# Performance work log

Hardware: AMD Instinct MI355X
Metric: run time of the kernel (lower is better)

Reference implementation:

```python
import jax, jax.numpy as jnp
import numpy as np

NUM_HEADS = 4


def setup_inputs() -> dict:
    key = jax.random.key(0)
    k1, k2, k3 = jax.random.split(key, 3)
    B, NN, C = 1, 256, 128
    x = jax.random.normal(k1, (B, NN, C), dtype=jnp.float32)
    # Linear(d_model, 4*d_model, bias=False); stored as (in, out) for x @ W_w
    W_w = jax.random.normal(k2, (C, 4 * C), dtype=jnp.float32) * (C ** -0.5)
    # proj = Linear(d_model, d_model) with bias; stored as (in, out)
    W_proj = jax.random.normal(k3, (C, C), dtype=jnp.float32) * (C ** -0.5)
    b_proj = jnp.zeros((C,), dtype=jnp.float32)
    return {"x": x, "W_w": W_w, "W_proj": W_proj, "b_proj": b_proj}


def reference(x, W_w, W_proj, b_proj):
    B, NN, C = x.shape
    H = NUM_HEADS
    D = C // H
    scale = D ** -0.5
    # qkv-style projection: (B, NN, 4, H, D) -> (4, B, H, NN, D)
    w = (x @ W_w).reshape(B, NN, 4, H, D).transpose(2, 0, 3, 1, 4)
    a, b, c, v = w[0], w[1], w[2], w[3]
    AB = jnp.einsum('bhid,bhjd->bhij', a, b) * scale
    CD = jnp.einsum('bhid,bhkd->bhik', a, c) * scale
    EF = jnp.einsum('bhjd,bhkd->bhjk', b, c) * scale
    # Triplet scores: (B, H, NN, NN, NN)
    A_ijk = AB[..., :, :, None] + CD[..., :, None, :] + EF[..., None, :, :]
    e = jnp.exp(A_ijk)
    # Normalize over (i, j) for each k, per original sum(dim=(-2,-3))
    norm = jnp.clip(e.sum(axis=(-2, -3), keepdims=True), 1e-6, None)
    en = e / norm
    x1 = jnp.einsum('bhijk,bhjd->bhid', en, v)
    x2 = jnp.einsum('bhijk,bhkd->bhid', en, v)
    out = (x1 * x2).transpose(0, 2, 1, 3).reshape(B, NN, C)
    return out @ W_proj + b_proj
```

## Files before the change

### kernel.cpp

```cpp
#include <hip/hip_runtime.h>
#include <hip/hip_bf16.h>


constexpr size_t OFF_W     = 0;
constexpr size_t OFF_P     = 131072;
constexpr size_t OFF_Q     = OFF_P + 262144;
constexpr size_t OFF_RT    = OFF_Q + 262144;
constexpr size_t OFF_T     = OFF_RT + 262144;
constexpr size_t OFF_S     = OFF_T + 524288;
constexpr size_t OFF_NORMP = OFF_S + 524288;

__global__ __launch_bounds__(256) void k_w(const float* __restrict__ x,
                                           const float* __restrict__ Ww,
                                           float* __restrict__ w,
                                           const float* __restrict__ bp,
                                           float* __restrict__ out) {
    __shared__ __align__(16) float As[1152];
    __shared__ __align__(16) float Bs[1152];
    int j0 = blockIdx.x * 32, i0 = blockIdx.y * 32;
    int t = threadIdx.x, tx = t & 15, ty = t >> 4, r = t >> 3, g = t & 7;
    {
        int oidx = (blockIdx.y * 16 + blockIdx.x) * 256 + t;
        out[oidx] = bp[oidx & 127];
    }
    float4 a4 = *(const float4*)&x[(size_t)(i0 + r) * 128 + g * 4];
    float4 b4 = *(const float4*)&Ww[(size_t)r * 512 + j0 + g * 4];
    float a00 = 0, a01 = 0, a10 = 0, a11 = 0;
    for (int kc = 0; kc < 128; kc += 32) {
        As[(g * 4 + 0) * 36 + r] = a4.x; As[(g * 4 + 1) * 36 + r] = a4.y;
        As[(g * 4 + 2) * 36 + r] = a4.z; As[(g * 4 + 3) * 36 + r] = a4.w;
        *(float4*)&Bs[r * 36 + g * 4] = b4;
        __syncthreads();
        if (kc + 32 < 128) {
            a4 = *(const float4*)&x[(size_t)(i0 + r) * 128 + kc + 32 + g * 4];
            b4 = *(const float4*)&Ww[(size_t)(kc + 32 + r) * 512 + j0 + g * 4];
        }
#pragma unroll
        for (int kk = 0; kk < 32; kk++) {
            float2 av = *(float2*)&As[kk * 36 + ty * 2];
            float2 bv = *(float2*)&Bs[kk * 36 + tx * 2];
            a00 += av.x * bv.x; a01 += av.x * bv.y;
            a10 += av.y * bv.x; a11 += av.y * bv.y;
        }
        __syncthreads();
    }
    *(float2*)&w[(size_t)(i0 + ty * 2) * 512 + j0 + tx * 2] = make_float2(a00, a01);
    *(float2*)&w[(size_t)(i0 + ty * 2 + 1) * 512 + j0 + tx * 2] = make_float2(a10, a11);
}

__global__ __launch_bounds__(256, 2) void k_T(const float* __restrict__ w,
                                              float* __restrict__ P,
                                              float* __restrict__ Q,
                                              float* __restrict__ Rt,
                                              float* __restrict__ T,
                                              float* __restrict__ normp) {
    __shared__ __align__(16) float aT[1152];
    __shared__ __align__(16) float cT[1152];
    __shared__ __align__(16) float bT[1152];
    __shared__ __align__(16) float PsT[1152];
    __shared__ __align__(16) float RsT[1152];
    int h = blockIdx.z >> 1, jh = blockIdx.z & 1;
    int k0 = blockIdx.x * 32, i0 = blockIdx.y * 32;
    int jc0 = jh * 128;
    size_t hb = (size_t)h * 65536;
    int t = threadIdx.x, tx = t & 15, ty = t >> 4, r = t >> 3, g = t & 7;
    const float sc = 0.17677669529663687f;

    float4 av = *(const float4*)&w[(size_t)(i0 + r) * 512 + h * 32 + g * 4];
    aT[(g * 4 + 0) * 36 + r] = av.x; aT[(g * 4 + 1) * 36 + r] = av.y;
    aT[(g * 4 + 2) * 36 + r] = av.z; aT[(g * 4 + 3) * 36 + r] = av.w;
    float4 cv = *(const float4*)&w[(size_t)(k0 + r) * 512 + 256 + h * 32 + g * 4];
    cT[(g * 4 + 0) * 36 + r] = cv.x; cT[(g * 4 + 1) * 36 + r] = cv.y;
    cT[(g * 4 + 2) * 36 + r] = cv.z; cT[(g * 4 + 3) * 36 + r] = cv.w;
    float4 bv = *(const float4*)&w[(size_t)(jc0 + r) * 512 + 128 + h * 32 + g * 4];
    __syncthreads();

    float2 a_tx[32], c_tx[32];
#pragma unroll
    for (int d = 0; d < 32; d++) {
        a_tx[d] = *(float2*)&aT[d * 36 + 2 * tx];
        c_tx[d] = *(float2*)&cT[d * 36 + 2 * tx];
    }

    float dq00 = 0, dq01 = 0, dq10 = 0, dq11 = 0;
#pragma unroll
    for (int d = 0; d < 32; d++) {
        float2 a2 = *(float2*)&aT[d * 36 + 2 * ty];
        float2 c2 = c_tx[d];
        dq00 += a2.x * c2.x; dq01 += a2.x * c2.y;
        dq10 += a2.y * c2.x; dq11 += a2.y * c2.y;
    }
    float q00 = __expf(sc * dq00), q01 = __expf(sc * dq01);
    float q10 = __expf(sc * dq10), q11 = __expf(sc * dq11);
    if (jh == 0) {
        *(float2*)&Q[hb + (size_t)(i0 + ty * 2) * 256 + k0 + tx * 2] = make_float2(q00, q01);
        *(float2*)&Q[hb + (size_t)(i0 + ty * 2 + 1) * 256 + k0 + tx * 2] = make_float2(q10, q11);
    }

    const bool wP = (k0 == 0), wR = (blockIdx.y == 0);
    float acc00 = 0, acc01 = 0, acc10 = 0, acc11 = 0;
    for (int jc = jc0; jc < jc0 + 128; jc += 32) {
        bT[(g * 4 + 0) * 36 + r] = bv.x; bT[(g * 4 + 1) * 36 + r] = bv.y;
        bT[(g * 4 + 2) * 36 + r] = bv.z; bT[(g * 4 + 3) * 36 + r] = bv.w;
        __syncthreads();
        if (jc + 32 < jc0 + 128)
            bv = *(const float4*)&w[(size_t)(jc + 32 + r) * 512 + 128 + h * 32 + g * 4];
        float dp00 = 0, dp01 = 0, dp10 = 0, dp11 = 0;
        float dr00 = 0, dr01 = 0, dr10 = 0, dr11 = 0;
#pragma unroll
        for (int d = 0; d < 32; d++) {
            float2 b2 = *(float2*)&bT[d * 36 + 2 * ty];
            float2 a2 = a_tx[d];
            float2 c2 = c_tx[d];
            dp00 += b2.x * a2.x; dp01 += b2.x * a2.y;
            dp10 += b2.y * a2.x; dp11 += b2.y * a2.y;
            dr00 += b2.x * c2.x; dr01 += b2.x * c2.y;
            dr10 += b2.y * c2.x; dr11 += b2.y * c2.y;
        }
        float p00 = __expf(sc * dp00), p01 = __expf(sc * dp01);
        float p10 = __expf(sc * dp10), p11 = __expf(sc * dp11);
        float r00 = __expf(sc * dr00), r01 = __expf(sc * dr01);
        float r10 = __expf(sc * dr10), r11 = __expf(sc * dr11);
        *(float2*)&PsT[(2 * tx + 0) * 36 + 2 * ty] = make_float2(p00, p10);
        *(float2*)&PsT[(2 * tx + 1) * 36 + 2 * ty] = make_float2(p01, p11);
        *(float2*)&RsT[(2 * tx + 0) * 36 + 2 * ty] = make_float2(r00, r10);
        *(float2*)&RsT[(2 * tx + 1) * 36 + 2 * ty] = make_float2(r01, r11);
        if (wP) {
            *(float2*)&P[hb + (size_t)(i0 + tx * 2 + 0) * 256 + jc + ty * 2] = make_float2(p00, p10);
            *(float2*)&P[hb + (size_t)(i0 + tx * 2 + 1) * 256 + jc + ty * 2] = make_float2(p01, p11);
        }
        if (wR) {
            *(float2*)&Rt[hb + (size_t)(k0 + tx * 2 + 0) * 256 + jc + ty * 2] = make_float2(r00, r10);
            *(float2*)&Rt[hb + (size_t)(k0 + tx * 2 + 1) * 256 + jc + ty * 2] = make_float2(r01, r11);
        }
        __syncthreads();
#pragma unroll
        for (int q = 0; q < 8; q++) {
            float4 pA = *(float4*)&PsT[(2 * ty + 0) * 36 + 4 * q];
            float4 pB = *(float4*)&PsT[(2 * ty + 1) * 36 + 4 * q];
            float4 rA = *(float4*)&RsT[(2 * tx + 0) * 36 + 4 * q];
            float4 rB = *(float4*)&RsT[(2 * tx + 1) * 36 + 4 * q];
            acc00 += pA.x * rA.x + pA.y * rA.y + pA.z * rA.z + pA.w * rA.w;
            acc01 += pA.x * rB.x + pA.y * rB.y + pA.z * rB.z + pA.w * rB.w;
            acc10 += pB.x * rA.x + pB.y * rA.y + pB.z * rA.z + pB.w * rA.w;
            acc11 += pB.x * rB.x + pB.y * rB.y + pB.z * rB.z + pB.w * rB.w;
        }
    }
    float* Tp = T + (size_t)jh * 262144;
    *(float2*)&Tp[hb + (size_t)(i0 + ty * 2) * 256 + k0 + tx * 2] = make_float2(acc00, acc01);
    *(float2*)&Tp[hb + (size_t)(i0 + ty * 2 + 1) * 256 + k0 + tx * 2] = make_float2(acc10, acc11);
    __syncthreads();
    float* red = PsT;
    red[ty * 34 + tx * 2]     = q00 * acc00 + q10 * acc10;
    red[ty * 34 + tx * 2 + 1] = q01 * acc01 + q11 * acc11;
    __syncthreads();
    if (t < 32) {
        float s = 0.f;
#pragma unroll
        for (int m = 0; m < 16; m++) s += red[m * 34 + t];
        normp[h * 4096 + (jh * 8 + blockIdx.y) * 256 + k0 + t] = s;
    }
}

__global__ __launch_bounds__(256, 2) void k_S(const float* __restrict__ Q,
                                              const float* __restrict__ Rt,
                                              const float* __restrict__ normp,
                                              float* __restrict__ S) {
    __shared__ __align__(16) float AsT[1152];
    __shared__ __align__(16) float BsT[1152];
    __shared__ float rn_s[256];
    int h = blockIdx.z >> 1, kh = blockIdx.z & 1;
    int j0 = blockIdx.x * 32, i0 = blockIdx.y * 32;
    int kc0 = kh * 128;
    size_t hb = (size_t)h * 65536;
    int t = threadIdx.x, tx = t & 15, ty = t >> 4, r = t >> 3, g = t & 7;
    {
        float s = 0.f;
#pragma unroll
        for (int ib = 0; ib < 16; ib++) s += normp[h * 4096 + ib * 256 + t];
        rn_s[t] = 1.f / fmaxf(s, 1e-6f);
    }
    float4 a4 = *(const float4*)&Q[hb + (size_t)(i0 + r) * 256 + kc0 + g * 4];
    float4 b4 = *(const float4*)&Rt[hb + (size_t)(kc0 + r) * 256 + j0 + g * 4];
    __syncthreads();
    float a00 = 0, a01 = 0, a10 = 0, a11 = 0;
    for (int kc = kc0; kc < kc0 + 128; kc += 32) {
        float4 rn4 = *(float4*)&rn_s[kc + g * 4];
        float4 as4;
        as4.x = a4.x * rn4.x; as4.y = a4.y * rn4.y;
        as4.z = a4.z * rn4.z; as4.w = a4.w * rn4.w;
        *(float4*)&AsT[r * 36 + g * 4] = as4;
        BsT[(g * 4 + 0) * 36 + r] = b4.x;
        BsT[(g * 4 + 1) * 36 + r] = b4.y;
        BsT[(g * 4 + 2) * 36 + r] = b4.z;
        BsT[(g * 4 + 3) * 36 + r] = b4.w;
        __syncthreads();
        if (kc + 32 < kc0 + 128) {
            a4 = *(const float4*)&Q[hb + (size_t)(i0 + r) * 256 + kc + 32 + g * 4];
            b4 = *(const float4*)&Rt[hb + (size_t)(kc + 32 + r) * 256 + j0 + g * 4];
        }
#pragma unroll
        for (int q = 0; q < 8; q++) {
            float4 aA = *(float4*)&AsT[(2 * ty + 0) * 36 + 4 * q];
            float4 aB = *(float4*)&AsT[(2 * ty + 1) * 36 + 4 * q];
            float4 bA = *(float4*)&BsT[(2 * tx + 0) * 36 + 4 * q];
            float4 bB = *(float4*)&BsT[(2 * tx + 1) * 36 + 4 * q];
            a00 += aA.x * bA.x + aA.y * bA.y + aA.z * bA.z + aA.w * bA.w;
            a01 += aA.x * bB.x + aA.y * bB.y + aA.z * bB.z + aA.w * bB.w;
            a10 += aB.x * bA.x + aB.y * bA.y + aB.z * bA.z + aB.w * bA.w;
            a11 += aB.x * bB.x + aB.y * bB.y + aB.z * bB.z + aB.w * bB.w;
        }
        __syncthreads();
    }
    float* Sp = S + (size_t)kh * 262144;
    *(float2*)&Sp[hb + (size_t)(i0 + ty * 2) * 256 + j0 + tx * 2] = make_float2(a00, a01);
    *(float2*)&Sp[hb + (size_t)(i0 + ty * 2 + 1) * 256 + j0 + tx * 2] = make_float2(a10, a11);
}

__global__ __launch_bounds__(256) void k_x1x2(
    const float* __restrict__ P, const float* __restrict__ Q,
    const float* __restrict__ S, const float* __restrict__ T,
    const float* __restrict__ normp, const float* __restrict__ w,
    const float* __restrict__ Wp, float* __restrict__ out) {
    int h = blockIdx.y;
    int i0 = blockIdx.x * 4;
    size_t hb = (size_t)h * 65536;
    __shared__ __align__(16) float wp[1024];
    __shared__ __align__(16) float wq[1024];
    __shared__ __align__(16) float vT[8320];
    __shared__ float rn_s[256];
    __shared__ float ys[144];
    int t = threadIdx.x;
    {
        float s = 0.f;
#pragma unroll
        for (int ib = 0; ib < 16; ib++) s += normp[h * 4096 + ib * 256 + t];
        rn_s[t] = 1.f / fmaxf(s, 1e-6f);
    }
    __syncthreads();
    {
        int rr = t >> 6, jj = (t & 63) * 4;
        size_t o = hb + (size_t)(i0 + rr) * 256 + jj;
        float4 p4  = *(const float4*)&P[o];
        float4 s4a = *(const float4*)&S[o];
        float4 s4b = *(const float4*)&S[o + 262144];
        float4 q4  = *(const float4*)&Q[o];
        float4 t4a = *(const float4*)&T[o];
        float4 t4b = *(const float4*)&T[o + 262144];
        float4 rn4 = *(float4*)&rn_s[jj];
        float4 wpv, wqv;
        wpv.x = p4.x * (s4a.x + s4b.x); wpv.y = p4.y * (s4a.y + s4b.y);
        wpv.z = p4.z * (s4a.z + s4b.z); wpv.w = p4.w * (s4a.w + s4b.w);
        wqv.x = q4.x * (t4a.x + t4b.x) * rn4.x;
        wqv.y = q4.y * (t4a.y + t4b.y) * rn4.y;
        wqv.z = q4.z * (t4a.z + t4b.z) * rn4.z;
        wqv.w = q4.w * (t4a.w + t4b.w) * rn4.w;
        *(float4*)&wp[rr * 256 + jj] = wpv;
        *(float4*)&wq[rr * 256 + jj] = wqv;
    }
#pragma unroll
    for (int m = 0; m < 8; m++) {
        int jj = m * 32 + (t >> 3);
        int dd = (t & 7) * 4;
        float4 v4 = *(const float4*)&w[(size_t)jj * 512 + 384 + h * 32 + dd];
        vT[(dd + 0) * 260 + jj] = v4.x;
        vT[(dd + 1) * 260 + jj] = v4.y;
        vT[(dd + 2) * 260 + jj] = v4.z;
        vT[(dd + 3) * 260 + jj] = v4.w;
    }
    __syncthreads();
    int d = t & 31, rl = (t >> 5) & 3, jh2 = t >> 7;
    int jbase = jh2 * 128;
    float x1 = 0.f, x2 = 0.f;
#pragma unroll
    for (int q = 0; q < 32; q++) {
        int j = jbase + 4 * q;
        float4 wp4 = *(float4*)&wp[rl * 256 + j];
        float4 wq4 = *(float4*)&wq[rl * 256 + j];
        float4 v4  = *(float4*)&vT[d * 260 + j];
        x1 += wp4.x * v4.x + wp4.y * v4.y + wp4.z * v4.z + wp4.w * v4.w;
        x2 += wq4.x * v4.x + wq4.y * v4.y + wq4.z * v4.z + wq4.w * v4.w;
    }
    __syncthreads();
    float* redx = wp;
    float* redy = wq;
    redx[t] = x1;
    redy[t] = x2;
    float* Wps = vT;
#pragma unroll
    for (int m = 0; m < 4; m++) {
        int idx = m * 256 + t;
        int k = idx >> 5, n = (idx & 31) * 4;
        *(float4*)&Wps[k * 128 + n] = *(const float4*)&Wp[(size_t)(h * 32 + k) * 128 + n];
    }
    __syncthreads();
    if (t < 128) {
        float x1t = redx[t] + redx[t + 128];
        float x2t = redy[t] + redy[t + 128];
        ys[rl * 33 + d] = x1t * x2t;
    }
    __syncthreads();
    int n = t & 127, ti = t >> 7;
    float acc0 = 0.f, acc1 = 0.f;
#pragma unroll
    for (int k = 0; k < 32; k++) {
        float wv = Wps[k * 128 + n];
        acc0 += ys[(ti + 0) * 33 + k] * wv;
        acc1 += ys[(ti + 2) * 33 + k] * wv;
    }
    atomicAdd(&out[(size_t)(i0 + ti + 0) * 128 + n], acc0);
    atomicAdd(&out[(size_t)(i0 + ti + 2) * 128 + n], acc1);
}

extern "C" void kernel_launch(void* const* d_in, const int* in_sizes, int n_in,
                              void* d_out, int out_size, void* d_ws, size_t ws_size,
                              hipStream_t stream) {
    const float* x      = (const float*)d_in[0];
    const float* W_w    = (const float*)d_in[1];
    const float* W_proj = (const float*)d_in[2];
    const float* b_proj = (const float*)d_in[3];
    float* out = (float*)d_out;
    float* ws  = (float*)d_ws;

    float* w     = ws + OFF_W;
    float* P     = ws + OFF_P;
    float* Q     = ws + OFF_Q;
    float* Rt    = ws + OFF_RT;
    float* T     = ws + OFF_T;
    float* S     = ws + OFF_S;
    float* normp = ws + OFF_NORMP;

    k_w<<<dim3(16, 8), 256, 0, stream>>>(x, W_w, w, b_proj, out);
    k_T<<<dim3(8, 8, 8), 256, 0, stream>>>(w, P, Q, Rt, T, normp);
    k_S<<<dim3(8, 8, 8), 256, 0, stream>>>(Q, Rt, normp, S);
    k_x1x2<<<dim3(64, 4), 256, 0, stream>>>(P, Q, S, T, normp, w, W_proj, out);
}
```

Before: 39.77 us.

## Fuse S matmul into x1x2 kernel, computing S rows on the fly

Removes the separate k_S GEMM launch and its S workspace round-trip. Each x1x2 block now computes its 4 rows of S = (Q*rn) @ Rt directly, splitting K across four thread groups and reducing through shared memory. It saves one launch and the S global writes and reads. In exchange every block streams the full per-head Rt (256x256) from global or L2 with little reuse, across 256 blocks.

```diff
diff --git a/kernel.cpp b/kernel.cpp
--- a/kernel.cpp
+++ b/kernel.cpp
@@ -7,8 +7,7 @@
 constexpr size_t OFF_Q     = OFF_P + 262144;
 constexpr size_t OFF_RT    = OFF_Q + 262144;
 constexpr size_t OFF_T     = OFF_RT + 262144;
-constexpr size_t OFF_S     = OFF_T + 524288;
-constexpr size_t OFF_NORMP = OFF_S + 524288;
+constexpr size_t OFF_NORMP = OFF_T + 524288;
 
 __global__ __launch_bounds__(256) void k_w(const float* __restrict__ x,
                                            const float* __restrict__ Ww,
@@ -162,73 +161,20 @@
     }
 }
 
-__global__ __launch_bounds__(256, 2) void k_S(const float* __restrict__ Q,
-                                              const float* __restrict__ Rt,
-                                              const float* __restrict__ normp,
-                                              float* __restrict__ S) {
-    __shared__ __align__(16) float AsT[1152];
-    __shared__ __align__(16) float BsT[1152];
-    __shared__ float rn_s[256];
-    int h = blockIdx.z >> 1, kh = blockIdx.z & 1;
-    int j0 = blockIdx.x * 32, i0 = blockIdx.y * 32;
-    int kc0 = kh * 128;
-    size_t hb = (size_t)h * 65536;
-    int t = threadIdx.x, tx = t & 15, ty = t >> 4, r = t >> 3, g = t & 7;
-    {
-        float s = 0.f;
-#pragma unroll
-        for (int ib = 0; ib < 16; ib++) s += normp[h * 4096 + ib * 256 + t];
-        rn_s[t] = 1.f / fmaxf(s, 1e-6f);
-    }
-    float4 a4 = *(const float4*)&Q[hb + (size_t)(i0 + r) * 256 + kc0 + g * 4];
-    float4 b4 = *(const float4*)&Rt[hb + (size_t)(kc0 + r) * 256 + j0 + g * 4];
-    __syncthreads();
-    float a00 = 0, a01 = 0, a10 = 0, a11 = 0;
-    for (int kc = kc0; kc < kc0 + 128; kc += 32) {
-        float4 rn4 = *(float4*)&rn_s[kc + g * 4];
-        float4 as4;
-        as4.x = a4.x * rn4.x; as4.y = a4.y * rn4.y;
-        as4.z = a4.z * rn4.z; as4.w = a4.w * rn4.w;
-        *(float4*)&AsT[r * 36 + g * 4] = as4;
-        BsT[(g * 4 + 0) * 36 + r] = b4.x;
-        BsT[(g * 4 + 1) * 36 + r] = b4.y;
-        BsT[(g * 4 + 2) * 36 + r] = b4.z;
-        BsT[(g * 4 + 3) * 36 + r] = b4.w;
-        __syncthreads();
-        if (kc + 32 < kc0 + 128) {
-            a4 = *(const float4*)&Q[hb + (size_t)(i0 + r) * 256 + kc + 32 + g * 4];
-            b4 = *(const float4*)&Rt[hb + (size_t)(kc + 32 + r) * 256 + j0 + g * 4];
-        }
-#pragma unroll
-        for (int q = 0; q < 8; q++) {
-            float4 aA = *(float4*)&AsT[(2 * ty + 0) * 36 + 4 * q];
-            float4 aB = *(float4*)&AsT[(2 * ty + 1) * 36 + 4 * q];
-            float4 bA = *(float4*)&BsT[(2 * tx + 0) * 36 + 4 * q];
-            float4 bB = *(float4*)&BsT[(2 * tx + 1) * 36 + 4 * q];
-            a00 += aA.x * bA.x + aA.y * bA.y + aA.z * bA.z + aA.w * bA.w;
-            a01 += aA.x * bB.x + aA.y * bB.y + aA.z * bB.z + aA.w * bB.w;
-            a10 += aB.x * bA.x + aB.y * bA.y + aB.z * bA.z + aB.w * bA.w;
-            a11 += aB.x * bB.x + aB.y * bB.y + aB.z * bB.z + aB.w * bB.w;
-        }
-        __syncthreads();
-    }
-    float* Sp = S + (size_t)kh * 262144;
-    *(float2*)&Sp[hb + (size_t)(i0 + ty * 2) * 256 + j0 + tx * 2] = make_float2(a00, a01);
-    *(float2*)&Sp[hb + (size_t)(i0 + ty * 2 + 1) * 256 + j0 + tx * 2] = make_float2(a10, a11);
-}
-
-__global__ __launch_bounds__(256) void k_x1x2(
+__global__ __launch_bounds__(256) void k_x1x2S(
     const float* __restrict__ P, const float* __restrict__ Q,
-    const float* __restrict__ S, const float* __restrict__ T,
+    const float* __restrict__ Rt, const float* __restrict__ T,
     const float* __restrict__ normp, const float* __restrict__ w,
     const float* __restrict__ Wp, float* __restrict__ out) {
     int h = blockIdx.y;
     int i0 = blockIdx.x * 4;
     size_t hb = (size_t)h * 65536;
+    __shared__ float rn_s[256];
+    __shared__ __align__(16) float qs[1024];
+    __shared__ __align__(16) float Ss[1024];
     __shared__ __align__(16) float wp[1024];
     __shared__ __align__(16) float wq[1024];
     __shared__ __align__(16) float vT[8320];
-    __shared__ float rn_s[256];
     __shared__ float ys[144];
     int t = threadIdx.x;
     {
@@ -239,25 +185,50 @@
     }
     __syncthreads();
     {
-        int rr = t >> 6, jj = (t & 63) * 4;
-        size_t o = hb + (size_t)(i0 + rr) * 256 + jj;
-        float4 p4  = *(const float4*)&P[o];
-        float4 s4a = *(const float4*)&S[o];
-        float4 s4b = *(const float4*)&S[o + 262144];
-        float4 q4  = *(const float4*)&Q[o];
-        float4 t4a = *(const float4*)&T[o];
-        float4 t4b = *(const float4*)&T[o + 262144];
-        float4 rn4 = *(float4*)&rn_s[jj];
-        float4 wpv, wqv;
-        wpv.x = p4.x * (s4a.x + s4b.x); wpv.y = p4.y * (s4a.y + s4b.y);
-        wpv.z = p4.z * (s4a.z + s4b.z); wpv.w = p4.w * (s4a.w + s4b.w);
-        wqv.x = q4.x * (t4a.x + t4b.x) * rn4.x;
-        wqv.y = q4.y * (t4a.y + t4b.y) * rn4.y;
-        wqv.z = q4.z * (t4a.z + t4b.z) * rn4.z;
-        wqv.w = q4.w * (t4a.w + t4b.w) * rn4.w;
-        *(float4*)&wp[rr * 256 + jj] = wpv;
-        *(float4*)&wq[rr * 256 + jj] = wqv;
-    }
+        int row = t >> 6, jq = (t & 63) * 4;
+        float4 q4 = *(const float4*)&Q[hb + (size_t)(i0 + row) * 256 + jq];
+        float4 rn4 = *(float4*)&rn_s[jq];
+        q4.x *= rn4.x; q4.y *= rn4.y; q4.z *= rn4.z; q4.w *= rn4.w;
+        *(float4*)&qs[row * 256 + jq] = q4;
+    }
+    __syncthreads();
+    {
+        int jq = (t & 63) * 4, kq = t >> 6;
+        float4 acc0 = {0, 0, 0, 0}, acc1 = {0, 0, 0, 0};
+        float4 acc2 = {0, 0, 0, 0}, acc3 = {0, 0, 0, 0};
+#pragma unroll 8
+        for (int kk = 0; kk < 64; kk++) {
+            int k = kq * 64 + kk;
+            float4 r4 = *(const float4*)&Rt[hb + (size_t)k * 256 + jq];
+            float q0 = qs[0 * 256 + k], q1 = qs[1 * 256 + k];
+            float q2 = qs[2 * 256 + k], q3 = qs[3 * 256 + k];
+            acc0.x += q0 * r4.x; acc0.y += q0 * r4.y; acc0.z += q0 * r4.z; acc0.w += q0 * r4.w;
+            acc1.x += q1 * r4.x; acc1.y += q1 * r4.y; acc1.z += q1 * r4.z; acc1.w += q1 * r4.w;
+            acc2.x += q2 * r4.x; acc2.y += q2 * r4.y; acc2.z += q2 * r4.z; acc2.w += q2 * r4.w;
+            acc3.x += q3 * r4.x; acc3.y += q3 * r4.y; acc3.z += q3 * r4.z; acc3.w += q3 * r4.w;
+        }
+        float* red = vT;
+        *(float4*)&red[(kq * 4 + 0) * 256 + jq] = acc0;
+        *(float4*)&red[(kq * 4 + 1) * 256 + jq] = acc1;
+        *(float4*)&red[(kq * 4 + 2) * 256 + jq] = acc2;
+        *(float4*)&red[(kq * 4 + 3) * 256 + jq] = acc3;
+    }
+    __syncthreads();
+    {
+        int row = t >> 6, jq = (t & 63) * 4;
+        float* red = vT;
+        float4 s0 = *(float4*)&red[(0 * 4 + row) * 256 + jq];
+        float4 s1 = *(float4*)&red[(1 * 4 + row) * 256 + jq];
+        float4 s2 = *(float4*)&red[(2 * 4 + row) * 256 + jq];
+        float4 s3 = *(float4*)&red[(3 * 4 + row) * 256 + jq];
+        float4 sm;
+        sm.x = (s0.x + s1.x) + (s2.x + s3.x);
+        sm.y = (s0.y + s1.y) + (s2.y + s3.y);
+        sm.z = (s0.z + s1.z) + (s2.z + s3.z);
+        sm.w = (s0.w + s1.w) + (s2.w + s3.w);
+        *(float4*)&Ss[row * 256 + jq] = sm;
+    }
+    __syncthreads();
 #pragma unroll
     for (int m = 0; m < 8; m++) {
         int jj = m * 32 + (t >> 3);
@@ -267,6 +238,22 @@
         vT[(dd + 1) * 260 + jj] = v4.y;
         vT[(dd + 2) * 260 + jj] = v4.z;
         vT[(dd + 3) * 260 + jj] = v4.w;
+    }
+    {
+        int rr = t >> 6, jj = (t & 63) * 4;
+        size_t o = hb + (size_t)(i0 + rr) * 256 + jj;
+        float4 p4  = *(const float4*)&P[o];
+        float4 t4a = *(const float4*)&T[o];
+        float4 t4b = *(const float4*)&T[o + 262144];
+        float4 q4  = *(float4*)&qs[rr * 256 + jj];
+        float4 s4  = *(float4*)&Ss[rr * 256 + jj];
+        float4 wpv, wqv;
+        wpv.x = p4.x * s4.x; wpv.y = p4.y * s4.y;
+        wpv.z = p4.z * s4.z; wpv.w = p4.w * s4.w;
+        wqv.x = q4.x * (t4a.x + t4b.x); wqv.y = q4.y * (t4a.y + t4b.y);
+        wqv.z = q4.z * (t4a.z + t4b.z); wqv.w = q4.w * (t4a.w + t4b.w);
+        *(float4*)&wp[rr * 256 + jj] = wpv;
+        *(float4*)&wq[rr * 256 + jj] = wqv;
     }
     __syncthreads();
     int d = t & 31, rl = (t >> 5) & 3, jh2 = t >> 7;
@@ -327,11 +314,9 @@
     float* Q     = ws + OFF_Q;
     float* Rt    = ws + OFF_RT;
     float* T     = ws + OFF_T;
-    float* S     = ws + OFF_S;
     float* normp = ws + OFF_NORMP;
 
     k_w<<<dim3(16, 8), 256, 0, stream>>>(x, W_w, w, b_proj, out);
     k_T<<<dim3(8, 8, 8), 256, 0, stream>>>(w, P, Q, Rt, T, normp);
-    k_S<<<dim3(8, 8, 8), 256, 0, stream>>>(Q, Rt, normp, S);
-    k_x1x2<<<dim3(64, 4), 256, 0, stream>>>(P, Q, S, T, normp, w, W_proj, out);
+    k_x1x2S<<<dim3(64, 4), 256, 0, stream>>>(P, Q, Rt, T, normp, w, W_proj, out);
 }
```

After: 36.52 us. -8.2%, faster.
